# Kernel tuning notes

Hardware: AMD Instinct MI355X
Metric: run time of the kernel (lower is better)

## Reference

```python
import jax, jax.numpy as jnp
import numpy as np

D_MODEL = 1024
N_HEADS = 16
D_HEAD = D_MODEL // N_HEADS
D_FF = 4096
B, T = 2, 2048


def setup_inputs() -> dict:
    key = jax.random.key(0)
    ks = jax.random.split(key, 7)
    s = lambda fan_in: 1.0 / np.sqrt(fan_in)
    return {
        "x": jax.random.normal(ks[0], (B, T, D_MODEL), dtype=jnp.float32),
        "ln1_g": jnp.ones((D_MODEL,), jnp.float32),
        "ln1_b": jnp.zeros((D_MODEL,), jnp.float32),
        "w_qkv": jax.random.normal(ks[1], (D_MODEL, 3 * D_MODEL), jnp.float32) * s(D_MODEL),
        "w_proj": jax.random.normal(ks[2], (D_MODEL, D_MODEL), jnp.float32) * s(D_MODEL),
        "ln2_g": jnp.ones((D_MODEL,), jnp.float32),
        "ln2_b": jnp.zeros((D_MODEL,), jnp.float32),
        "w_fc1": jax.random.normal(ks[3], (D_MODEL, D_FF), jnp.float32) * s(D_MODEL),
        "w_fc2": jax.random.normal(ks[4], (D_FF, D_MODEL), jnp.float32) * s(D_FF),
    }


def _layernorm(x, g, b, eps=1e-5):
    mu = jnp.mean(x, axis=-1, keepdims=True)
    var = jnp.var(x, axis=-1, keepdims=True)
    return (x - mu) * jax.lax.rsqrt(var + eps) * g + b


def _attn(x, w_qkv, w_proj):
    Bx, Tx, d = x.shape
    qkv = x @ w_qkv  # [B,T,3d]
    q, k, v = jnp.split(qkv, 3, axis=-1)
    split = lambda t: t.reshape(Bx, Tx, N_HEADS, D_HEAD).transpose(0, 2, 1, 3)
    q, k, v = split(q), split(k), split(v)
    scores = jnp.einsum("bhqd,bhkd->bhqk", q, k) / np.sqrt(D_HEAD).astype(np.float32)
    mask = jnp.tril(jnp.ones((Tx, Tx), dtype=bool))
    scores = jnp.where(mask, scores, -jnp.inf)
    attn = jax.nn.softmax(scores, axis=-1)
    out = jnp.einsum("bhqk,bhkd->bhqd", attn, v)
    out = out.transpose(0, 2, 1, 3).reshape(Bx, Tx, d)
    return out @ w_proj


def reference(x, ln1_g, ln1_b, w_qkv, w_proj, ln2_g, ln2_b, w_fc1, w_fc2):
    x = x + _attn(_layernorm(x, ln1_g, ln1_b), w_qkv, w_proj)
    h = jax.nn.gelu(_layernorm(x, ln2_g, ln2_b) @ w_fc1, approximate=False)
    return x + h @ w_fc2
```

## Files before the change

### kernel.cpp

```cpp
#include <hip/hip_runtime.h>
#include <math.h>

using short8 = __attribute__((ext_vector_type(8))) short;
using f32x4  = __attribute__((ext_vector_type(4))) float;
typedef unsigned short ushort;

__device__ inline ushort f2bf(float f) {
    union { float f; unsigned int i; } v; v.f = f;
    unsigned int x = v.i;
    return (ushort)((x + 0x7FFFu + ((x >> 16) & 1u)) >> 16);
}
__device__ inline ushort f2bf_hu(float f) {
    union { float f; unsigned int i; } v; v.f = f;
    return (ushort)((v.i + 0x8000u) >> 16);
}
__device__ inline void st_out(float* p, float v) { *p = v; }
__device__ inline void st_out(ushort* p, float v) { *p = f2bf(v); }

__device__ inline void gl_lds16(const ushort* g, ushort* l) {
    __builtin_amdgcn_global_load_lds((const __attribute__((address_space(1))) unsigned int*)g,
                                     (__attribute__((address_space(3))) unsigned int*)l, 16, 0, 0);
}
#define MFMA __builtin_amdgcn_mfma_f32_16x16x32_bf16

__global__ __launch_bounds__(256) void ln_kernel(const float* __restrict__ x,
                                                 const float* __restrict__ g,
                                                 const float* __restrict__ b,
                                                 ushort* __restrict__ y) {
    int row = blockIdx.x;
    const float* xr = x + (size_t)row * 1024;
    int t = threadIdx.x;
    float v[4];
    float s = 0.f, s2 = 0.f;
#pragma unroll
    for (int i = 0; i < 4; i++) {
        v[i] = xr[t + i * 256];
        s += v[i]; s2 += v[i] * v[i];
    }
#pragma unroll
    for (int off = 1; off < 64; off <<= 1) {
        s += __shfl_xor(s, off); s2 += __shfl_xor(s2, off);
    }
    __shared__ float ps[8];
    int w = t >> 6;
    if ((t & 63) == 0) { ps[w] = s; ps[4 + w] = s2; }
    __syncthreads();
    s  = ps[0] + ps[1] + ps[2] + ps[3];
    s2 = ps[4] + ps[5] + ps[6] + ps[7];
    float mu   = s * (1.0f / 1024.0f);
    float var  = s2 * (1.0f / 1024.0f) - mu * mu;
    float rinv = rsqrtf(var + 1e-5f);
    ushort* yr = y + (size_t)row * 1024;
#pragma unroll
    for (int i = 0; i < 4; i++) {
        int c = t + i * 256;
        yr[c] = f2bf((v[i] - mu) * rinv * g[c] + b[c]);
    }
}

__global__ __launch_bounds__(256) void wt_kernel(const float* __restrict__ s,
                                                 ushort* __restrict__ d, int K, int N) {
    __shared__ float tile[32][33];
    int n0 = blockIdx.x * 32, k0 = blockIdx.y * 32;
    int tx = threadIdx.x & 31, ty = threadIdx.x >> 5;
#pragma unroll
    for (int i = 0; i < 4; i++)
        tile[ty + i * 8][tx] = s[(size_t)(k0 + ty + i * 8) * N + n0 + tx];
    __syncthreads();
#pragma unroll
    for (int i = 0; i < 4; i++)
        d[(size_t)(n0 + ty + i * 8) * K + k0 + tx] = f2bf(tile[tx][ty + i * 8]);
}

template <int EPI, typename CT>
__global__ __launch_bounds__(256) void gemm_kernel(const ushort* __restrict__ A,
                                                   const ushort* __restrict__ Bt,
                                                   CT* __restrict__ C,
                                                   const float* __restrict__ R,
                                                   ushort* __restrict__ VT,
                                                   int M, int N, int K) {
    __shared__ alignas(16) ushort As[128 * 64];
    __shared__ alignas(16) ushort Bs[128 * 64];
    int t = threadIdx.x, lane = t & 63, w = t >> 6;
    int bm = blockIdx.y * 128, bn = blockIdx.x * 128;
    int wm = (w >> 1) * 64, wn = (w & 1) * 64;
    f32x4 acc[4][4] = {};
    int srow = lane >> 3;
    int schunk = (lane & 7) ^ (lane >> 3);
    int rs = lane & 15, qd = lane >> 4;

    for (int k0 = 0; k0 < K; k0 += 64) {
        __syncthreads();
#pragma unroll
        for (int i = 0; i < 4; i++) {
            int rr = w * 32 + i * 8;
            gl_lds16(A  + (size_t)(bm + rr + srow) * K + k0 + schunk * 8, &As[rr * 64]);
            gl_lds16(Bt + (size_t)(bn + rr + srow) * K + k0 + schunk * 8, &Bs[rr * 64]);
        }
        __syncthreads();
#pragma unroll
        for (int half = 0; half < 2; half++) {
            int cq = qd + half * 4;
            short8 af[4], bf[4];
#pragma unroll
            for (int i = 0; i < 4; i++) {
                int ml = wm + i * 16 + rs;
                af[i] = *(const short8*)&As[ml * 64 + ((cq ^ (ml & 7)) * 8)];
                int nl = wn + i * 16 + rs;
                bf[i] = *(const short8*)&Bs[nl * 64 + ((cq ^ (nl & 7)) * 8)];
            }
#pragma unroll
            for (int mi = 0; mi < 4; mi++)
#pragma unroll
                for (int ni = 0; ni < 4; ni++)
                    acc[mi][ni] = MFMA(af[mi], bf[ni], acc[mi][ni], 0, 0, 0);
        }
    }
#pragma unroll
    for (int mi = 0; mi < 4; mi++)
#pragma unroll
        for (int ni = 0; ni < 4; ni++) {
            int row = bm + wm + mi * 16 + qd * 4;
            int col = bn + wn + ni * 16 + rs;
            if (EPI == 3) {
                if (col < 2048) {
                    float sc = (col < 1024) ? 0.125f : 1.0f;
#pragma unroll
                    for (int r = 0; r < 4; r++)
                        ((ushort*)C)[(size_t)(row + r) * 2048 + col] = f2bf(acc[mi][ni][r] * sc);
                } else {
                    int rel = col - 2048, hh = rel >> 6, dd = rel & 63;
                    ushort tmp[4];
#pragma unroll
                    for (int r = 0; r < 4; r++) tmp[r] = f2bf(acc[mi][ni][r]);
                    size_t base = ((size_t)((row >> 11) * 16 + hh) * 64 + dd) * 2048 + (row & 2047);
                    *(uint2*)&VT[base] = *(uint2*)tmp;
                }
            } else {
#pragma unroll
                for (int r = 0; r < 4; r++) {
                    float v = acc[mi][ni][r];
                    size_t idx = (size_t)(row + r) * N + col;
                    if (EPI == 1) v += R[idx];
                    if (EPI == 2) v = 0.5f * v * (1.0f + erff(v * 0.70710678118f));
                    st_out(&C[idx], v);
                }
            }
        }
}

template <int EPI, typename CT>
__global__ __launch_bounds__(256) void gemm_n64_kernel(const ushort* __restrict__ A,
                                                       const ushort* __restrict__ Bt,
                                                       CT* __restrict__ C,
                                                       const float* __restrict__ R,
                                                       int M, int N, int K, int Kh) {
    __shared__ alignas(16) ushort As[128 * 64];
    __shared__ alignas(16) ushort Bs[64 * 64];
    int t = threadIdx.x, lane = t & 63, w = t >> 6;
    int bm = blockIdx.x * 128, bn = blockIdx.y * 64;
    int kbeg = blockIdx.z * Kh;
    int wm = (w >> 1) * 64, wn = (w & 1) * 32;
    f32x4 acc[4][2] = {};
    int srow = lane >> 3;
    int schunk = (lane & 7) ^ (lane >> 3);
    int rs = lane & 15, qd = lane >> 4;

    for (int k0 = kbeg; k0 < kbeg + Kh; k0 += 64) {
        __syncthreads();
#pragma unroll
        for (int i = 0; i < 4; i++) {
            int rr = w * 32 + i * 8;
            gl_lds16(A + (size_t)(bm + rr + srow) * K + k0 + schunk * 8, &As[rr * 64]);
        }
#pragma unroll
        for (int i = 0; i < 2; i++) {
            int rr = w * 16 + i * 8;
            gl_lds16(Bt + (size_t)(bn + rr + srow) * K + k0 + schunk * 8, &Bs[rr * 64]);
        }
        __syncthreads();
#pragma unroll
        for (int half = 0; half < 2; half++) {
            int cq = qd + half * 4;
            short8 af[4], bfr[2];
#pragma unroll
            for (int i = 0; i < 4; i++) {
                int ml = wm + i * 16 + rs;
                af[i] = *(const short8*)&As[ml * 64 + ((cq ^ (ml & 7)) * 8)];
            }
#pragma unroll
            for (int j = 0; j < 2; j++) {
                int nl = wn + j * 16 + rs;
                bfr[j] = *(const short8*)&Bs[nl * 64 + ((cq ^ (nl & 7)) * 8)];
            }
#pragma unroll
            for (int mi = 0; mi < 4; mi++)
#pragma unroll
                for (int ni = 0; ni < 2; ni++)
                    acc[mi][ni] = MFMA(af[mi], bfr[ni], acc[mi][ni], 0, 0, 0);
        }
    }
#pragma unroll
    for (int mi = 0; mi < 4; mi++)
#pragma unroll
        for (int ni = 0; ni < 2; ni++) {
            int row = bm + wm + mi * 16 + qd * 4;
            int col = bn + wn + ni * 16 + rs;
#pragma unroll
            for (int r = 0; r < 4; r++) {
                float v = acc[mi][ni][r];
                size_t idx = (size_t)(row + r) * N + col;
                if (EPI == 4) {
                    atomicAdd((float*)&C[idx], v);
                } else {
                    if (EPI == 1) v += R[idx];
                    st_out(&C[idx], v);
                }
            }
        }
}

__global__ __launch_bounds__(256) void attn_kernel(const ushort* __restrict__ qk,
                                                   const ushort* __restrict__ vT,
                                                   ushort* __restrict__ attnO,
                                                   float* __restrict__ pO,
                                                   float* __restrict__ pL) {
    __shared__ alignas(16) ushort Ks[128 * 64];
    __shared__ alignas(16) ushort VTs[64 * 128];
    int t = threadIdx.x, lane = t & 63, w = t >> 6;
    int p = blockIdx.x, bh = blockIdx.y, z = blockIdx.z;
    int bb = bh >> 4, h = bh & 15;
    const ushort* qkb = qk + (size_t)bb * 2048 * 2048;
    const ushort* qptr = qkb + h * 64;
    const ushort* kptr = qkb + 1024 + h * 64;
    const ushort* vtb  = vT + (size_t)bh * 64 * 2048;
    int rs = lane & 15, qd = lane >> 4;
    int krl = lane >> 3, kch = lane & 7;
    int vrl = lane >> 4, vch = lane & 15;
    int nkA = p / 2 + 1, nkB = (31 - p) / 2 + 1;
    int qts[2] = {p, 31 - p};
    int nks[2] = {nkA, nkB};
    int kb[2], ke[2];
    if (z == 0) { kb[0] = 0; ke[0] = nkA; kb[1] = 0;       ke[1] = 9 - nkA; }
    else        { kb[0] = 0; ke[0] = 0;   kb[1] = 9 - nkA; ke[1] = nkB;     }
    ushort* Pw = &Ks[w * 2048];

    for (int ph = 0; ph < 2; ph++) {
        if (kb[ph] >= ke[ph]) continue;
        int qt = qts[ph], nk = nks[ph];
        int q0 = qt * 64;
        int qrow = q0 + w * 16 + rs;
        short8 aq0 = *(const short8*)(qptr + (size_t)qrow * 2048 + qd * 8);
        short8 aq1 = *(const short8*)(qptr + (size_t)qrow * 2048 + 32 + qd * 8);
        int myq = q0 + w * 16 + qd * 4;
        f32x4 o_acc[4] = {};
        float l_part[4] = {0.f, 0.f, 0.f, 0.f};

        for (int kt = kb[ph]; kt < ke[ph]; kt++) {
            int k0 = kt * 128;
            __syncthreads();
#pragma unroll
            for (int i = 0; i < 4; i++) {
                int kk = w * 32 + i * 8 + krl;
                gl_lds16(kptr + (size_t)(k0 + kk) * 2048 + ((kch ^ (kk & 7)) * 8), &Ks[(w * 32 + i * 8) * 64]);
                int dd = w * 16 + i * 4 + vrl;
                gl_lds16(vtb + (size_t)dd * 2048 + k0 + ((vch ^ (dd & 15)) * 8), &VTs[(w * 16 + i * 4) * 128]);
            }
            __syncthreads();
            f32x4 s[8];
#pragma unroll
            for (int c = 0; c < 8; c++) {
                int kk = c * 16 + rs;
                short8 kf0 = *(const short8*)&Ks[kk * 64 + ((qd ^ (kk & 7)) * 8)];
                short8 kf1 = *(const short8*)&Ks[kk * 64 + (((qd + 4) ^ (kk & 7)) * 8)];
                f32x4 zz = {};
                zz = MFMA(aq0, kf0, zz, 0, 0, 0);
                zz = MFMA(aq1, kf1, zz, 0, 0, 0);
                s[c] = zz;
            }
            bool lastt = (kt == nk - 1);
#pragma unroll
            for (int c = 0; c < 8; c++) {
                int kk = k0 + c * 16 + rs;
#pragma unroll
                for (int r = 0; r < 4; r++) {
                    float pv = __expf(s[c][r]);
                    if (lastt && (kk > myq + r)) pv = 0.f;
                    s[c][r] = pv;
                    l_part[r] += pv;
                }
            }
            __syncthreads();
#pragma unroll
            for (int r = 0; r < 4; r++) {
                int row = qd * 4 + r;
#pragma unroll
                for (int c = 0; c < 8; c++) {
                    int chunk = c * 2 + (rs >> 3);
                    Pw[row * 128 + ((chunk ^ row) * 8) + (rs & 7)] = f2bf_hu(s[c][r]);
                }
            }
            short8 ap[4];
#pragma unroll
            for (int kc = 0; kc < 4; kc++)
                ap[kc] = *(const short8*)&Pw[rs * 128 + (((kc * 4 + qd) ^ rs) * 8)];
#pragma unroll
            for (int dt = 0; dt < 4; dt++) {
                int dd = dt * 16 + rs;
#pragma unroll
                for (int kc = 0; kc < 4; kc++) {
                    int g = kc * 4 + qd;
                    short8 bv = *(const short8*)&VTs[dd * 128 + ((g ^ (dd & 15)) * 8)];
                    o_acc[dt] = MFMA(ap[kc], bv, o_acc[dt], 0, 0, 0);
                }
            }
        }
#pragma unroll
        for (int r = 0; r < 4; r++)
#pragma unroll
            for (int off = 1; off < 16; off <<= 1)
                l_part[r] += __shfl_xor(l_part[r], off);
        if (ph == 0) {
#pragma unroll
            for (int dt = 0; dt < 4; dt++)
#pragma unroll
                for (int r = 0; r < 4; r++)
                    attnO[(size_t)(bb * 2048 + myq + r) * 1024 + h * 64 + dt * 16 + rs] =
                        f2bf(o_acc[dt][r] / l_part[r]);
        } else {
            int qb16 = 15 - p;
            size_t ob = ((size_t)(z * 32 + bh) * 16 + qb16) * 4096;
#pragma unroll
            for (int dt = 0; dt < 4; dt++)
#pragma unroll
                for (int r = 0; r < 4; r++)
                    pO[ob + (size_t)(w * 16 + qd * 4 + r) * 64 + dt * 16 + rs] = o_acc[dt][r];
            if (rs == 0)
#pragma unroll
                for (int r = 0; r < 4; r++)
                    pL[((size_t)(z * 32 + bh) * 16 + qb16) * 64 + w * 16 + qd * 4 + r] = l_part[r];
        }
    }
}

__global__ __launch_bounds__(256) void attn_comb_kernel(const float* __restrict__ pO,
                                                        const float* __restrict__ pL,
                                                        ushort* __restrict__ attnO) {
    int idx4 = (blockIdx.x * 256 + threadIdx.x) * 4;
    int dim = idx4 & 63, row = (idx4 >> 6) & 63, qb = (idx4 >> 12) & 15, bh = idx4 >> 16;
    float4 o0 = *(const float4*)(pO + idx4);
    float4 o1 = *(const float4*)(pO + 2097152 + idx4);
    float inv = 1.0f / (pL[idx4 >> 6] + pL[32768 + (idx4 >> 6)]);
    int grow = (bh >> 4) * 2048 + (16 + qb) * 64 + row;
    int col = (bh & 15) * 64 + dim;
    ushort r4[4] = { f2bf((o0.x + o1.x) * inv), f2bf((o0.y + o1.y) * inv),
                     f2bf((o0.z + o1.z) * inv), f2bf((o0.w + o1.w) * inv) };
    *(uint2*)(attnO + (size_t)grow * 1024 + col) = *(uint2*)r4;
}

extern "C" void kernel_launch(void* const* d_in, const int* in_sizes, int n_in,
                              void* d_out, int out_size, void* d_ws, size_t ws_size,
                              hipStream_t stream) {
    const float* x     = (const float*)d_in[0];
    const float* ln1g  = (const float*)d_in[1];
    const float* ln1b  = (const float*)d_in[2];
    const float* wqkv  = (const float*)d_in[3];
    const float* wproj = (const float*)d_in[4];
    const float* ln2g  = (const float*)d_in[5];
    const float* ln2b  = (const float*)d_in[6];
    const float* wfc1  = (const float*)d_in[7];
    const float* wfc2  = (const float*)d_in[8];
    float* out = (float*)d_out;
    char* ws = (char*)d_ws;
    const size_t MB = 1024 * 1024;

    ushort* wbufA = (ushort*)(ws);
    ushort* lnbuf = (ushort*)(ws + 8 * MB);
    ushort* qk    = (ushort*)(ws + 16 * MB);
    ushort* vT    = (ushort*)(ws + 32 * MB);
    float*  pL    = (float*)(ws + 40 * MB);
    const int Rr = 4096;

    ln_kernel<<<Rr, 256, 0, stream>>>(x, ln1g, ln1b, lnbuf);
    wt_kernel<<<dim3(3072 / 32, 1024 / 32), 256, 0, stream>>>(wqkv, wbufA, 1024, 3072);
    gemm_kernel<3, ushort><<<dim3(3072 / 128, Rr / 128), 256, 0, stream>>>(lnbuf, wbufA, qk, nullptr, vT, Rr, 3072, 1024);
    attn_kernel<<<dim3(16, 32, 2), 256, 0, stream>>>(qk, vT, lnbuf, out, pL);
    attn_comb_kernel<<<2048, 256, 0, stream>>>(out, pL, lnbuf);
    wt_kernel<<<dim3(1024 / 32, 1024 / 32), 256, 0, stream>>>(wproj, wbufA, 1024, 1024);
    gemm_n64_kernel<1, float><<<dim3(Rr / 128, 1024 / 64, 1), 256, 0, stream>>>(lnbuf, wbufA, out, x, Rr, 1024, 1024, 1024);
    ln_kernel<<<Rr, 256, 0, stream>>>(out, ln2g, ln2b, lnbuf);
    wt_kernel<<<dim3(4096 / 32, 1024 / 32), 256, 0, stream>>>(wfc1, wbufA, 1024, 4096);

    if (ws_size >= 56 * MB) {
        ushort* hmid  = qk;
        ushort* wbufB = (ushort*)(ws + 48 * MB);
        wt_kernel<<<dim3(1024 / 32, 4096 / 32), 256, 0, stream>>>(wfc2, wbufB, 4096, 1024);
        gemm_kernel<2, ushort><<<dim3(4096 / 128, Rr / 128), 256, 0, stream>>>(lnbuf, wbufA, hmid, nullptr, nullptr, Rr, 4096, 1024);
        gemm_n64_kernel<4, float><<<dim3(Rr / 128, 1024 / 64, 2), 256, 0, stream>>>(hmid, wbufB, out, nullptr, Rr, 1024, 4096, 2048);
    } else {
        ushort* hmid  = qk;
        ushort* wbufB = (ushort*)(ws + 32 * MB);
        wt_kernel<<<dim3(1024 / 32, 4096 / 32), 256, 0, stream>>>(wfc2, wbufB, 4096, 1024);
        for (int hf = 0; hf < 2; hf++) {
            const ushort* lnh = lnbuf + (size_t)hf * 2048 * 1024;
            float* outh = out + (size_t)hf * 2048 * 1024;
            gemm_kernel<2, ushort><<<dim3(4096 / 128, 2048 / 128), 256, 0, stream>>>(lnh, wbufA, hmid, nullptr, nullptr, 2048, 4096, 1024);
            gemm_n64_kernel<4, float><<<dim3(2048 / 128, 1024 / 64, 2), 256, 0, stream>>>(hmid, wbufB, outh, nullptr, 2048, 1024, 4096, 2048);
        }
    }
}
```

Baseline: 368.9 us.

## Stage GEMM epilogue through LDS for coalesced stores and use fast GELU

The bf16-output GEMM now writes its accumulator tile into swizzled shared memory, then emits 16-byte coalesced row stores instead of per-element 2-byte scattered stores. The V-transpose tiles take an early-return path. The exact erf GELU is replaced by a tanh-style sigmoid approximation built on __expf and a hardware reciprocal. This targets store inefficiency and the transcendental cost in the epilogue, at the cost of extra syncs and a slight numerical deviation from exact GELU.

```diff
diff --git a/kernel.cpp b/kernel.cpp
--- a/kernel.cpp
+++ b/kernel.cpp
@@ -22,6 +22,13 @@
                                      (__attribute__((address_space(3))) unsigned int*)l, 16, 0, 0);
 }
 #define MFMA __builtin_amdgcn_mfma_f32_16x16x32_bf16
+
+__device__ inline float gelu_fast(float x) {
+    float t2 = x * x;
+    float y  = x * fmaf(t2, 0.07135481f, 1.5957691f);
+    float e  = __expf(y);
+    return x * e * __builtin_amdgcn_rcpf(e + 1.0f);
+}
 
 __global__ __launch_bounds__(256) void ln_kernel(const float* __restrict__ x,
                                                  const float* __restrict__ g,
@@ -72,15 +79,15 @@
         d[(size_t)(n0 + ty + i * 8) * K + k0 + tx] = f2bf(tile[tx][ty + i * 8]);
 }
 
-template <int EPI, typename CT>
+template <int EPI>
 __global__ __launch_bounds__(256) void gemm_kernel(const ushort* __restrict__ A,
                                                    const ushort* __restrict__ Bt,
-                                                   CT* __restrict__ C,
-                                                   const float* __restrict__ R,
+                                                   ushort* __restrict__ C,
                                                    ushort* __restrict__ VT,
                                                    int M, int N, int K) {
-    __shared__ alignas(16) ushort As[128 * 64];
-    __shared__ alignas(16) ushort Bs[128 * 64];
+    __shared__ alignas(16) ushort SMEM[128 * 128];
+    ushort* As = SMEM;
+    ushort* Bs = SMEM + 128 * 64;
     int t = threadIdx.x, lane = t & 63, w = t >> 6;
     int bm = blockIdx.y * 128, bn = blockIdx.x * 128;
     int wm = (w >> 1) * 64, wn = (w & 1) * 64;
@@ -116,37 +123,50 @@
                     acc[mi][ni] = MFMA(af[mi], bf[ni], acc[mi][ni], 0, 0, 0);
         }
     }
+
+    if (EPI == 3 && bn >= 2048) {
+#pragma unroll
+        for (int mi = 0; mi < 4; mi++)
+#pragma unroll
+            for (int ni = 0; ni < 4; ni++) {
+                int row = bm + wm + mi * 16 + qd * 4;
+                int col = bn + wn + ni * 16 + rs;
+                int rel = col - 2048, hh = rel >> 6, dd = rel & 63;
+                ushort tmp[4];
+#pragma unroll
+                for (int r = 0; r < 4; r++) tmp[r] = f2bf(acc[mi][ni][r]);
+                size_t base = ((size_t)((row >> 11) * 16 + hh) * 64 + dd) * 2048 + (row & 2047);
+                *(uint2*)&VT[base] = *(uint2*)tmp;
+            }
+        return;
+    }
+
+    float sc = (EPI == 3 && bn < 1024) ? 0.125f : 1.0f;
+    __syncthreads();
 #pragma unroll
     for (int mi = 0; mi < 4; mi++)
 #pragma unroll
         for (int ni = 0; ni < 4; ni++) {
-            int row = bm + wm + mi * 16 + qd * 4;
-            int col = bn + wn + ni * 16 + rs;
-            if (EPI == 3) {
-                if (col < 2048) {
-                    float sc = (col < 1024) ? 0.125f : 1.0f;
-#pragma unroll
-                    for (int r = 0; r < 4; r++)
-                        ((ushort*)C)[(size_t)(row + r) * 2048 + col] = f2bf(acc[mi][ni][r] * sc);
-                } else {
-                    int rel = col - 2048, hh = rel >> 6, dd = rel & 63;
-                    ushort tmp[4];
-#pragma unroll
-                    for (int r = 0; r < 4; r++) tmp[r] = f2bf(acc[mi][ni][r]);
-                    size_t base = ((size_t)((row >> 11) * 16 + hh) * 64 + dd) * 2048 + (row & 2047);
-                    *(uint2*)&VT[base] = *(uint2*)tmp;
-                }
-            } else {
-#pragma unroll
-                for (int r = 0; r < 4; r++) {
-                    float v = acc[mi][ni][r];
-                    size_t idx = (size_t)(row + r) * N + col;
-                    if (EPI == 1) v += R[idx];
-                    if (EPI == 2) v = 0.5f * v * (1.0f + erff(v * 0.70710678118f));
-                    st_out(&C[idx], v);
-                }
-            }
-        }
+            int lcolc = (wn + ni * 16 + rs) >> 3;
+            int lcolo = rs & 7;
+#pragma unroll
+            for (int r = 0; r < 4; r++) {
+                int row = wm + mi * 16 + qd * 4 + r;
+                float v = acc[mi][ni][r];
+                if (EPI == 2) v = gelu_fast(v);
+                if (EPI == 3) v *= sc;
+                SMEM[row * 128 + ((lcolc ^ (row & 15)) * 8) + lcolo] = f2bf(v);
+            }
+        }
+    __syncthreads();
+    int ldC = (EPI == 3) ? 2048 : N;
+#pragma unroll
+    for (int ps = 0; ps < 8; ps++) {
+        int row = ps * 16 + (t >> 4);
+        int c = t & 15;
+        short8 vv = *(const short8*)&SMEM[row * 128 + ((c ^ (row & 15)) * 8)];
+        *(short8*)(C + (size_t)(bm + row) * ldC + bn + c * 8) = vv;
+    }
 }
 
 template <int EPI, typename CT>
@@ -383,7 +403,7 @@
 
     ln_kernel<<<Rr, 256, 0, stream>>>(x, ln1g, ln1b, lnbuf);
     wt_kernel<<<dim3(3072 / 32, 1024 / 32), 256, 0, stream>>>(wqkv, wbufA, 1024, 3072);
-    gemm_kernel<3, ushort><<<dim3(3072 / 128, Rr / 128), 256, 0, stream>>>(lnbuf, wbufA, qk, nullptr, vT, Rr, 3072, 1024);
+    gemm_kernel<3><<<dim3(3072 / 128, Rr / 128), 256, 0, stream>>>(lnbuf, wbufA, qk, vT, Rr, 3072, 1024);
     attn_kernel<<<dim3(16, 32, 2), 256, 0, stream>>>(qk, vT, lnbuf, out, pL);
     attn_comb_kernel<<<2048, 256, 0, stream>>>(out, pL, lnbuf);
     wt_kernel<<<dim3(1024 / 32, 1024 / 32), 256, 0, stream>>>(wproj, wbufA, 1024, 1024);
@@ -395,7 +415,7 @@
         ushort* hmid  = qk;
         ushort* wbufB = (ushort*)(ws + 48 * MB);
         wt_kernel<<<dim3(1024 / 32, 4096 / 32), 256, 0, stream>>>(wfc2, wbufB, 4096, 1024);
-        gemm_kernel<2, ushort><<<dim3(4096 / 128, Rr / 128), 256, 0, stream>>>(lnbuf, wbufA, hmid, nullptr, nullptr, Rr, 4096, 1024);
+        gemm_kernel<2><<<dim3(4096 / 128, Rr / 128), 256, 0, stream>>>(lnbuf, wbufA, hmid, nullptr, Rr, 4096, 1024);
         gemm_n64_kernel<4, float><<<dim3(Rr / 128, 1024 / 64, 2), 256, 0, stream>>>(hmid, wbufB, out, nullptr, Rr, 1024, 4096, 2048);
     } else {
         ushort* hmid  = qk;
@@ -404,7 +424,7 @@
         for (int hf = 0; hf < 2; hf++) {
             const ushort* lnh = lnbuf + (size_t)hf * 2048 * 1024;
             float* outh = out + (size_t)hf * 2048 * 1024;
-            gemm_kernel<2, ushort><<<dim3(4096 / 128, 2048 / 128), 256, 0, stream>>>(lnh, wbufA, hmid, nullptr, nullptr, 2048, 4096, 1024);
+            gemm_kernel<2><<<dim3(4096 / 128, 2048 / 128), 256, 0, stream>>>(lnh, wbufA, hmid, nullptr, 2048, 4096, 1024);
             gemm_n64_kernel<4, float><<<dim3(2048 / 128, 1024 / 64, 2), 256, 0, stream>>>(hmid, wbufB, outh, nullptr, 2048, 1024, 4096, 2048);
         }
     }
```

Result: faster. 359.7 us (-2.5%).
